# Performance work log

Hardware: AMD Instinct MI355X
Metric: run time of the kernel (lower is better)

## Reference

```python
import jax, jax.numpy as jnp
import numpy as np

B, S, D, V = 64, 16, 2048, 128000


def setup_inputs() -> dict:
    key = jax.random.key(0)
    k1, k2, k3, k4, k5 = jax.random.split(key, 5)
    embedding = jax.random.normal(k1, (V, D), dtype=jnp.float32) * 0.02
    hidden_states = jax.random.normal(k2, (B, S, D), dtype=jnp.float32)
    output_positions = jnp.array([S - 1], dtype=jnp.int32)  # sample from last position
    temperatures = jax.random.uniform(k3, (B,), dtype=jnp.float32, minval=0.5, maxval=1.5)
    top_ps = jax.random.uniform(k4, (B,), dtype=jnp.float32, minval=0.7, maxval=1.0)
    top_ks = jax.random.randint(k5, (B,), 1, 64).astype(jnp.int32)
    return {
        "embedding": embedding,
        "hidden_states": hidden_states,
        "output_positions": output_positions,
        "temperatures": temperatures,
        "top_ps": top_ps,
        "top_ks": top_ks,
    }


def reference(embedding, hidden_states, output_positions, temperatures, top_ps, top_ks):
    # select output position: [B, S, D] -> [B, D]
    hs = jnp.take(hidden_states, output_positions, axis=1)[:, 0, :]
    # vocab logits: [B, V]
    logits = jnp.einsum("bd,vd->bv", hs, embedding)
    logits = logits / temperatures[:, None]
    probs = jax.nn.softmax(logits.astype(jnp.float32), axis=-1)
    # descending sort of probs
    order = jnp.argsort(-probs, axis=-1)                       # [B, V]
    probs_sort = jnp.take_along_axis(probs, order, axis=-1)    # [B, V] descending
    cum = jnp.cumsum(probs_sort, axis=-1)
    # top-p: zero everything whose exclusive-prefix mass exceeds top_p
    probs_sort = jnp.where((cum - probs_sort) > top_ps[:, None], 0.0, probs_sort)
    # top-k: keep only first top_k sorted entries
    ranks = jnp.arange(V, dtype=jnp.int32)[None, :]
    probs_sort = jnp.where(ranks >= top_ks[:, None], 0.0, probs_sort)
    # renormalize
    probs_sort = probs_sort / jnp.sum(probs_sort, axis=-1, keepdims=True)
    # scatter back to original vocab order via inverse permutation
    inv = jnp.argsort(order, axis=-1)
    probs_final = jnp.take_along_axis(probs_sort, inv, axis=-1)
    # multinomial sampling (one token per row); zeros -> log 0 = -inf, excluded
    skey = jax.random.key(42)
    next_token_ids = jax.random.categorical(skey, jnp.log(probs_final), axis=-1)
    return next_token_ids
```

## Files before the change

kernel.cpp:

```cpp
#include <hip/hip_runtime.h>
#include <math.h>

#define BATCH 64
#define SEQ 16
#define DIM 2048
#define VOCAB 128000

#define BM 64
#define BN 128
#define BK 32
#define NT (DIM / BK)
#define ASZ (BM * BK)
#define BSZ (BN * BK)

typedef __attribute__((ext_vector_type(8))) short bf16x8;
typedef __attribute__((ext_vector_type(4))) float f32x4;

__device__ __forceinline__ unsigned cvt_pk_bf16(float a, float b) {
  unsigned r;
  asm("v_cvt_pk_bf16_f32 %0, %1, %2" : "=v"(r) : "v"(a), "v"(b));
  return r;
}

__device__ __forceinline__ void split8(float4 x0, float4 x1, bf16x8* hi, bf16x8* lo) {
  float f[8] = {x0.x, x0.y, x0.z, x0.w, x1.x, x1.y, x1.z, x1.w};
  union { unsigned u[4]; bf16x8 v; } H, L;
#pragma unroll
  for (int w = 0; w < 4; ++w) {
    float a = f[2 * w], b = f[2 * w + 1];
    unsigned hp = cvt_pk_bf16(a, b);
    float ha = __uint_as_float(hp << 16);
    float hb = __uint_as_float(hp & 0xffff0000u);
    H.u[w] = hp;
    L.u[w] = cvt_pk_bf16(a - ha, b - hb);
  }
  *hi = H.v;
  *lo = L.v;
}

__device__ __forceinline__ void gload_lds16(const float* src, float* lds_dst) {
  __builtin_amdgcn_global_load_lds(
      (const __attribute__((address_space(1))) void*)src,
      (__attribute__((address_space(3))) void*)lds_dst, 16, 0, 0);
}

__global__ __launch_bounds__(256, 3) void logits_kernel(
    const float* __restrict__ emb,
    const float* __restrict__ hs,
    const int* __restrict__ pos,
    const float* __restrict__ temps,
    float* __restrict__ logits) {
  __shared__ float ldsA[2 * ASZ];
  __shared__ float ldsB[2 * BSZ];

  const int tid = threadIdx.x;
  const int lane = tid & 63;
  const int wid = tid >> 6;
  const int lrow = lane & 15;
  const int lkb = lane >> 4;
  const int vb = blockIdx.x * BN + wid * 32;
  const int p = pos[0];

  const int r8 = (lane >> 3) & 7;
  const int c8 = lane & 7;
  const int cswz = 4 * (c8 ^ r8);

  const float* aSrc[2];
  float* aDst[2];
#pragma unroll
  for (int q = 0; q < 2; ++q) {
    const int g = wid * 2 + q;
    const int R = g * 8 + r8;
    aSrc[q] = hs + ((size_t)R * SEQ + p) * DIM + cswz;
    aDst[q] = &ldsA[g * 8 * BK];
  }
  const float* bSrc[4];
  float* bDst[4];
#pragma unroll
  for (int q = 0; q < 4; ++q) {
    const int g = wid * 4 + q;
    const int R = g * 8 + r8;
    bSrc[q] = emb + (size_t)(blockIdx.x * BN + R) * DIM + cswz;
    bDst[q] = &ldsB[g * 8 * BK];
  }

  f32x4 acc[4][2];
#pragma unroll
  for (int i = 0; i < 4; ++i)
#pragma unroll
    for (int j = 0; j < 2; ++j) acc[i][j] = (f32x4){0.f, 0.f, 0.f, 0.f};

  const int sfr = 4 * (lrow & 7);
  const int off0 = (lkb * 8) ^ sfr;
  const int off1 = off0 ^ 4;

#define STAGE(T, BUF)                                                        \
  do {                                                                       \
    const int kof_ = (T) * BK;                                               \
    const int ao_ = (BUF) * ASZ;                                             \
    const int bo_ = (BUF) * BSZ;                                             \
    _Pragma("unroll")                                                        \
    for (int q = 0; q < 2; ++q) gload_lds16(aSrc[q] + kof_, aDst[q] + ao_);  \
    _Pragma("unroll")                                                        \
    for (int q = 0; q < 4; ++q) gload_lds16(bSrc[q] + kof_, bDst[q] + bo_);  \
  } while (0)

  STAGE(0, 0);
  STAGE(1, 1);

  for (int t = 0; t < NT; ++t) {
    const int cur = t & 1;
    if (t < NT - 1) {
      asm volatile("s_waitcnt vmcnt(6)" ::: "memory");
    } else {
      asm volatile("s_waitcnt vmcnt(0)" ::: "memory");
    }
    __builtin_amdgcn_sched_barrier(0);
    __builtin_amdgcn_s_barrier();

    const float* A = &ldsA[cur * ASZ];
    const float* B = &ldsB[cur * BSZ];
    float4 ra[4][2], rb[2][2];
#pragma unroll
    for (int i = 0; i < 4; ++i) {
      const float* rbase = &A[(16 * i + lrow) * BK];
      ra[i][0] = *(const float4*)(rbase + off0);
      ra[i][1] = *(const float4*)(rbase + off1);
    }
#pragma unroll
    for (int j = 0; j < 2; ++j) {
      const float* rbase = &B[(wid * 32 + 16 * j + lrow) * BK];
      rb[j][0] = *(const float4*)(rbase + off0);
      rb[j][1] = *(const float4*)(rbase + off1);
    }
    asm volatile("s_waitcnt lgkmcnt(0)" ::: "memory");
    __builtin_amdgcn_sched_barrier(0);
    __builtin_amdgcn_s_barrier();

    if (t + 2 < NT) STAGE(t + 2, cur);

    bf16x8 ah[4], al[4], bh[2], bl[2];
#pragma unroll
    for (int i = 0; i < 4; ++i) split8(ra[i][0], ra[i][1], &ah[i], &al[i]);
#pragma unroll
    for (int j = 0; j < 2; ++j) split8(rb[j][0], rb[j][1], &bh[j], &bl[j]);
#pragma unroll
    for (int i = 0; i < 4; ++i)
#pragma unroll
      for (int j = 0; j < 2; ++j) {
        acc[i][j] = __builtin_amdgcn_mfma_f32_16x16x32_bf16(ah[i], bh[j], acc[i][j], 0, 0, 0);
        acc[i][j] = __builtin_amdgcn_mfma_f32_16x16x32_bf16(ah[i], bl[j], acc[i][j], 0, 0, 0);
        acc[i][j] = __builtin_amdgcn_mfma_f32_16x16x32_bf16(al[i], bh[j], acc[i][j], 0, 0, 0);
      }
  }
#undef STAGE

#pragma unroll
  for (int i = 0; i < 4; ++i)
#pragma unroll
    for (int r = 0; r < 4; ++r) {
      const int b = 16 * i + lkb * 4 + r;
      const float tt = temps[b];
#pragma unroll
      for (int j = 0; j < 2; ++j) {
        const int v = vb + 16 * j + lrow;
        logits[(size_t)b * VOCAB + v] = acc[i][j][r] / tt;
      }
    }
}

__device__ __forceinline__ void threefry2x32(unsigned k0, unsigned k1,
                                             unsigned x0, unsigned x1,
                                             unsigned* o0, unsigned* o1) {
  const unsigned k2 = k0 ^ k1 ^ 0x1BD11BDAu;
  const unsigned ks[3] = {k0, k1, k2};
  const int rotA[4] = {13, 15, 26, 6};
  const int rotB[4] = {17, 29, 16, 24};
  x0 += k0;
  x1 += k1;
#pragma unroll
  for (int i = 0; i < 5; ++i) {
    const int* rr = (i & 1) ? rotB : rotA;
#pragma unroll
    for (int q = 0; q < 4; ++q) {
      x0 += x1;
      x1 = (x1 << rr[q]) | (x1 >> (32 - rr[q]));
      x1 ^= x0;
    }
    x0 += ks[(i + 1) % 3];
    x1 += ks[(i + 2) % 3] + (unsigned)(i + 1);
  }
  *o0 = x0;
  *o1 = x1;
}

__device__ float gumbel_noise(unsigned flat) {
  unsigned o0, o1;
  threefry2x32(0u, 42u, 0u, flat, &o0, &o1);
  unsigned bits = o0 ^ o1;
  unsigned fb = (bits >> 9) | 0x3f800000u;
  float u = __uint_as_float(fb) - 1.0f;
  const float tiny = 1.17549435e-38f;
  u = fmaxf(u, tiny);
  return -logf(-logf(u));
}

#define CAP 4096
#define NL 12
#define NTH 1024
#define NWAVE 16

__device__ __forceinline__ unsigned sortkey(float x) {
  unsigned bits = __float_as_uint(x);
  return (bits & 0x80000000u) ? ~bits : (bits | 0x80000000u);
}
__device__ __forceinline__ float inv_sortkey(unsigned u) {
  unsigned bits = (u & 0x80000000u) ? (u & 0x7fffffffu) : ~u;
  return __uint_as_float(bits);
}

__global__ __launch_bounds__(NTH) void sample_kernel(
    const float* __restrict__ logits,
    const float* __restrict__ top_ps,
    const int* __restrict__ top_ks,
    const float* __restrict__ temps,
    const int* __restrict__ pos,
    int ws_ok,
    int* __restrict__ out) {
  const int b = blockIdx.x;
  const int tid = threadIdx.x;
  const int lane = tid & 63;
  const int wave = tid >> 6;
  const float* row = logits + (size_t)b * VOCAB;
  const float4* row4 = (const float4*)row;
  const int N4 = VOCAB / 4;

  __shared__ float sred[NWAVE];
  __shared__ int scnt_sh[NL];
  __shared__ float smax, sz;
  __shared__ float sdelta;
  __shared__ unsigned scnt;
  __shared__ unsigned ubuf[CAP];
  __shared__ unsigned ibuf[CAP];
  __shared__ unsigned sorted_u[64];
  __shared__ unsigned sorted_i[64];

  const float D[NL] = {0.5f, 0.75f, 1.0f, 1.25f, 1.5f, 1.75f,
                       2.0f, 2.5f, 3.0f, 4.0f, 8.0f, 1e30f};

  float lmax = -__builtin_huge_valf();
  for (int i = tid; i < N4; i += NTH) {
    float4 v = row4[i];
    lmax = fmaxf(fmaxf(lmax, v.x), fmaxf(fmaxf(v.y, v.z), v.w));
  }
#pragma unroll
  for (int s = 32; s > 0; s >>= 1) lmax = fmaxf(lmax, __shfl_xor(lmax, s, 64));
  if (lane == 0) sred[wave] = lmax;
  if (tid < NL) scnt_sh[tid] = 0;
  __syncthreads();
  if (tid == 0) {
    float m = sred[0];
#pragma unroll
    for (int w = 1; w < NWAVE; ++w) m = fmaxf(m, sred[w]);
    smax = m;
  }
  __syncthreads();
  const float maxl = smax;

  float zsum = 0.f;
  int cnt[NL];
#pragma unroll
  for (int r = 0; r < NL; ++r) cnt[r] = 0;
  for (int i = tid; i < N4; i += NTH) {
    float4 v = row4[i];
    float xs[4] = {v.x, v.y, v.z, v.w};
#pragma unroll
    for (int c = 0; c < 4; ++c) {
      float x = xs[c];
      zsum += expf(x - maxl);
      float d = maxl - x;
#pragma unroll
      for (int r = 0; r < NL; ++r) cnt[r] += (d <= D[r]) ? 1 : 0;
    }
  }
#pragma unroll
  for (int s = 32; s > 0; s >>= 1) {
    zsum += __shfl_xor(zsum, s, 64);
#pragma unroll
    for (int r = 0; r < NL; ++r) cnt[r] += __shfl_xor(cnt[r], s, 64);
  }
  if (lane == 0) {
    sred[wave] = zsum;
#pragma unroll
    for (int r = 0; r < NL; ++r) atomicAdd(&scnt_sh[r], cnt[r]);
  }
  __syncthreads();
  if (tid == 0) {
    float z = 0.f;
#pragma unroll
    for (int w = 0; w < NWAVE; ++w) z += sred[w];
    sz = z;
    float dd = 1e30f;
#pragma unroll
    for (int r = NL - 1; r >= 0; --r)
      if (scnt_sh[r] >= 64) dd = D[r];
    sdelta = dd;
    scnt = 0;
  }
  __syncthreads();
  const float Z = sz;
  const float thrv = maxl - sdelta;

  for (int i = tid; i < N4; i += NTH) {
    float4 v = row4[i];
    float xs[4] = {v.x, v.y, v.z, v.w};
#pragma unroll
    for (int c = 0; c < 4; ++c) {
      if (xs[c] >= thrv) {
        unsigned slot = atomicAdd(&scnt, 1u);
        if (slot < CAP) {
          ubuf[slot] = sortkey(xs[c]);
          ibuf[slot] = (unsigned)(i * 4 + c);
        }
      }
    }
  }
  __syncthreads();
  const int n = (int)(scnt < (unsigned)CAP ? scnt : (unsigned)CAP);

  if (tid < 64) { sorted_u[tid] = 0u; sorted_i[tid] = 0u; }
  __syncthreads();
  for (int c = tid; c < n; c += NTH) {
    unsigned u = ubuf[c], idx = ibuf[c];
    int rank = 0;
    for (int j = 0; j < n; ++j) {
      unsigned uj = ubuf[j];
      rank += (uj > u) || (uj == u && ibuf[j] < idx);
    }
    if (rank < 64) { sorted_u[rank] = u; sorted_i[rank] = idx; }
  }
  __syncthreads();

  if (tid == 0) {
    const float topp = top_ps[b];
    const int k = top_ks[b];
    const float tval = temps[b];
    float cum = 0.f;
    float best = -__builtin_huge_valf();
    int bestidx = 0;
    for (int r = 0; r < 64 && r < n; ++r) {
      float x = inv_sortkey(sorted_u[r]);
      float pr = expf(x - maxl) / Z;
      cum += pr;
      bool keep = (r < k) && !((cum - pr) > topp) && (pr > 0.f);
      if (keep) {
        float g = gumbel_noise((unsigned)b * (unsigned)VOCAB + sorted_i[r]);
        float sc = x + g;
        if (sc > best) { best = sc; bestidx = (int)sorted_i[r]; }
      }
    }
    int token = bestidx;

    unsigned kat0, kat1;
    threefry2x32(0u, 0u, 0u, 0u, &kat0, &kat1);
    bool inputs_ok = (pos[0] >= 0 && pos[0] < SEQ) &&
                     (tval > 0.45f && tval < 1.55f) &&
                     (topp > 0.65f && topp <= 1.0f) &&
                     (k >= 1 && k < 64);
    if (!inputs_ok) token = 3333333;
    else if (!ws_ok) token = 7777777;
    else if (kat0 != 0x6b200159u || kat1 != 0x99ba4efeu) token = 5555555;
    else if (scnt > (unsigned)CAP || n < 64) token = 4444444;
    out[b] = token;
  }
}

extern "C" void kernel_launch(void* const* d_in, const int* in_sizes, int n_in,
                              void* d_out, int out_size, void* d_ws, size_t ws_size,
                              hipStream_t stream) {
  const float* emb   = (const float*)d_in[0];
  const float* hs    = (const float*)d_in[1];
  const int*   pos   = (const int*)d_in[2];
  const float* temps = (const float*)d_in[3];
  const float* topps = (const float*)d_in[4];
  const int*   topks = (const int*)d_in[5];
  float* logits = (float*)d_ws;
  int* out = (int*)d_out;

  const size_t need = (size_t)BATCH * VOCAB * sizeof(float);
  const int ws_ok = (ws_size >= need) ? 1 : 0;

  hipLaunchKernelGGL(logits_kernel, dim3(VOCAB / BN), dim3(256), 0, stream,
                     emb, hs, pos, temps, logits);
  hipLaunchKernelGGL(sample_kernel, dim3(BATCH), dim3(NTH), 0, stream,
                     logits, topps, topks, temps, pos, ws_ok, out);
}
```

Before: 330.3 us.

## Double BK, use 8 waves per block, and remap blocks across XCDs

The logits GEMM now uses a K-tile of 64 and 512 threads per block, so each wave covers 16 vocab columns instead of 32. The LDS swizzle and load addressing are rewritten to match. Block indices are remapped so that consecutive vocab tiles land on the same XCD, which aims to improve L2 locality for the shared hidden-state rows. The goal is fewer barriers per K and more memory-level parallelism in streaming the embedding, at the cost of more LDS per block and less register reuse of A fragments per wave.

```diff
diff --git a/kernel.cpp b/kernel.cpp
--- a/kernel.cpp
+++ b/kernel.cpp
@@ -8,10 +8,11 @@
 
 #define BM 64
 #define BN 128
-#define BK 32
+#define BK 64
 #define NT (DIM / BK)
 #define ASZ (BM * BK)
 #define BSZ (BN * BK)
+#define NXCD 8
 
 typedef __attribute__((ext_vector_type(8))) short bf16x8;
 typedef __attribute__((ext_vector_type(4))) float f32x4;
@@ -44,7 +45,7 @@
       (__attribute__((address_space(3))) void*)lds_dst, 16, 0, 0);
 }
 
-__global__ __launch_bounds__(256, 3) void logits_kernel(
+__global__ __launch_bounds__(512, 2) void logits_kernel(
     const float* __restrict__ emb,
     const float* __restrict__ hs,
     const int* __restrict__ pos,
@@ -58,41 +59,38 @@
   const int wid = tid >> 6;
   const int lrow = lane & 15;
   const int lkb = lane >> 4;
-  const int vb = blockIdx.x * BN + wid * 32;
   const int p = pos[0];
 
-  const int r8 = (lane >> 3) & 7;
-  const int c8 = lane & 7;
-  const int cswz = 4 * (c8 ^ r8);
+  const int blk = (blockIdx.x & 7) * 125 + (blockIdx.x >> 3);
+  const int vb = blk * BN + wid * 16;
+
+  const int rq = lane >> 4;
+  const int c16 = lane & 15;
 
   const float* aSrc[2];
   float* aDst[2];
 #pragma unroll
   for (int q = 0; q < 2; ++q) {
-    const int g = wid * 2 + q;
-    const int R = g * 8 + r8;
-    aSrc[q] = hs + ((size_t)R * SEQ + p) * DIM + cswz;
-    aDst[q] = &ldsA[g * 8 * BK];
+    const int row = wid * 8 + q * 4 + rq;
+    const int sc = (c16 & 8) | ((c16 ^ (row & 7)) & 7);
+    aSrc[q] = hs + ((size_t)row * SEQ + p) * DIM + 4 * sc;
+    aDst[q] = &ldsA[(wid * 8 + q * 4) * BK];
   }
   const float* bSrc[4];
   float* bDst[4];
 #pragma unroll
   for (int q = 0; q < 4; ++q) {
-    const int g = wid * 4 + q;
-    const int R = g * 8 + r8;
-    bSrc[q] = emb + (size_t)(blockIdx.x * BN + R) * DIM + cswz;
-    bDst[q] = &ldsB[g * 8 * BK];
-  }
-
-  f32x4 acc[4][2];
-#pragma unroll
-  for (int i = 0; i < 4; ++i)
-#pragma unroll
-    for (int j = 0; j < 2; ++j) acc[i][j] = (f32x4){0.f, 0.f, 0.f, 0.f};
-
-  const int sfr = 4 * (lrow & 7);
-  const int off0 = (lkb * 8) ^ sfr;
-  const int off1 = off0 ^ 4;
+    const int row = wid * 16 + q * 4 + rq;
+    const int sc = (c16 & 8) | ((c16 ^ (row & 7)) & 7);
+    bSrc[q] = emb + (size_t)(blk * BN + row) * DIM + 4 * sc;
+    bDst[q] = &ldsB[(wid * 16 + q * 4) * BK];
+  }
+
+  f32x4 acc[4];
+#pragma unroll
+  for (int i = 0; i < 4; ++i) acc[i] = (f32x4){0.f, 0.f, 0.f, 0.f};
+
+  const int co = 4 * (((lkb << 1) ^ (lrow & 7)) & 7);
 
 #define STAGE(T, BUF)                                                        \
   do {                                                                       \
@@ -120,18 +118,23 @@
 
     const float* A = &ldsA[cur * ASZ];
     const float* B = &ldsB[cur * BSZ];
-    float4 ra[4][2], rb[2][2];
+    float4 ra[4][2][2], rb[2][2];
 #pragma unroll
     for (int i = 0; i < 4; ++i) {
       const float* rbase = &A[(16 * i + lrow) * BK];
-      ra[i][0] = *(const float4*)(rbase + off0);
-      ra[i][1] = *(const float4*)(rbase + off1);
-    }
-#pragma unroll
-    for (int j = 0; j < 2; ++j) {
-      const float* rbase = &B[(wid * 32 + 16 * j + lrow) * BK];
-      rb[j][0] = *(const float4*)(rbase + off0);
-      rb[j][1] = *(const float4*)(rbase + off1);
+#pragma unroll
+      for (int s = 0; s < 2; ++s) {
+        ra[i][s][0] = *(const float4*)(rbase + s * 32 + co);
+        ra[i][s][1] = *(const float4*)(rbase + s * 32 + (co ^ 4));
+      }
+    }
+    {
+      const float* rbase = &B[(wid * 16 + lrow) * BK];
+#pragma unroll
+      for (int s = 0; s < 2; ++s) {
+        rb[s][0] = *(const float4*)(rbase + s * 32 + co);
+        rb[s][1] = *(const float4*)(rbase + s * 32 + (co ^ 4));
+      }
     }
     asm volatile("s_waitcnt lgkmcnt(0)" ::: "memory");
     __builtin_amdgcn_sched_barrier(0);
@@ -139,19 +142,19 @@
 
     if (t + 2 < NT) STAGE(t + 2, cur);
 
-    bf16x8 ah[4], al[4], bh[2], bl[2];
-#pragma unroll
-    for (int i = 0; i < 4; ++i) split8(ra[i][0], ra[i][1], &ah[i], &al[i]);
-#pragma unroll
-    for (int j = 0; j < 2; ++j) split8(rb[j][0], rb[j][1], &bh[j], &bl[j]);
-#pragma unroll
-    for (int i = 0; i < 4; ++i)
-#pragma unroll
-      for (int j = 0; j < 2; ++j) {
-        acc[i][j] = __builtin_amdgcn_mfma_f32_16x16x32_bf16(ah[i], bh[j], acc[i][j], 0, 0, 0);
-        acc[i][j] = __builtin_amdgcn_mfma_f32_16x16x32_bf16(ah[i], bl[j], acc[i][j], 0, 0, 0);
-        acc[i][j] = __builtin_amdgcn_mfma_f32_16x16x32_bf16(al[i], bh[j], acc[i][j], 0, 0, 0);
-      }
+#pragma unroll
+    for (int s = 0; s < 2; ++s) {
+      bf16x8 ah[4], al[4], bh, bl;
+#pragma unroll
+      for (int i = 0; i < 4; ++i) split8(ra[i][s][0], ra[i][s][1], &ah[i], &al[i]);
+      split8(rb[s][0], rb[s][1], &bh, &bl);
+#pragma unroll
+      for (int i = 0; i < 4; ++i) {
+        acc[i] = __builtin_amdgcn_mfma_f32_16x16x32_bf16(ah[i], bh, acc[i], 0, 0, 0);
+        acc[i] = __builtin_amdgcn_mfma_f32_16x16x32_bf16(ah[i], bl, acc[i], 0, 0, 0);
+        acc[i] = __builtin_amdgcn_mfma_f32_16x16x32_bf16(al[i], bh, acc[i], 0, 0, 0);
+      }
+    }
   }
 #undef STAGE
 
@@ -161,11 +164,8 @@
     for (int r = 0; r < 4; ++r) {
       const int b = 16 * i + lkb * 4 + r;
       const float tt = temps[b];
-#pragma unroll
-      for (int j = 0; j < 2; ++j) {
-        const int v = vb + 16 * j + lrow;
-        logits[(size_t)b * VOCAB + v] = acc[i][j][r] / tt;
-      }
+      const int v = vb + lrow;
+      logits[(size_t)b * VOCAB + v] = acc[i][r] / tt;
     }
 }
 
@@ -390,7 +390,7 @@
   const size_t need = (size_t)BATCH * VOCAB * sizeof(float);
   const int ws_ok = (ws_size >= need) ? 1 : 0;
 
-  hipLaunchKernelGGL(logits_kernel, dim3(VOCAB / BN), dim3(256), 0, stream,
+  hipLaunchKernelGGL(logits_kernel, dim3(VOCAB / BN), dim3(512), 0, stream,
                      emb, hs, pos, temps, logits);
   hipLaunchKernelGGL(sample_kernel, dim3(BATCH), dim3(NTH), 0, stream,
                      logits, topps, topks, temps, pos, ws_ok, out);
```

New measurement: 360.1 us. 1.09x slower.
